# Kernel optimization log

Measured on AMD Instinct MI355X. Metric: run time of the kernel, lower is better.

Reference implementation:

```python
import jax, jax.numpy as jnp
import numpy as np
from jax import lax

N_BOXES = 6000
IOU_THR = 0.5
CONF_THR = 0.6


def setup_inputs() -> dict:
    key = jax.random.key(0)
    k1, k2, k3 = jax.random.split(key, 3)
    # valid xyxy boxes: top-left in [0,1000), width/height in [1,101)
    xy = jax.random.uniform(k1, (N_BOXES, 2), dtype=jnp.float32) * 1000.0
    wh = jax.random.uniform(k2, (N_BOXES, 2), dtype=jnp.float32) * 100.0 + 1.0
    boxes = jnp.concatenate([xy, xy + wh], axis=-1)  # [N,4] x1,y1,x2,y2
    scores = jax.random.uniform(k3, (N_BOXES,), dtype=jnp.float32)
    return {"boxes": boxes, "scores": scores}


def _pairwise_iou(b):
    # b: [N,4] xyxy. Returns [N,N] IoU, coordinates handled separately to
    # avoid materializing [N,N,2] intermediates.
    x1, y1, x2, y2 = b[:, 0], b[:, 1], b[:, 2], b[:, 3]
    area = (x2 - x1) * (y2 - y1)  # [N]
    iw = jnp.clip(jnp.minimum(x2[:, None], x2[None, :]) - jnp.maximum(x1[:, None], x1[None, :]), 0.0)
    ih = jnp.clip(jnp.minimum(y2[:, None], y2[None, :]) - jnp.maximum(y1[:, None], y1[None, :]), 0.0)
    inter = iw * ih  # [N,N]
    return inter / (area[:, None] + area[None, :] - inter)


def reference(boxes, scores):
    """torchvision-style NMS (suppress IoU > 0.5) then confidence filter (>= 0.6).
    Returns masked scores [N]: score where the box survives both stages, else 0.
    (Fixed-shape mask form of the original index outputs, for jit compatibility.)
    """
    n = scores.shape[0]
    order = jnp.argsort(-scores)  # descending by confidence
    iou = _pairwise_iou(boxes[order])  # [N,N] in sorted order
    idx = jnp.arange(n)

    def body(suppressed, i):
        keep_i = jnp.logical_not(suppressed[i])
        # a kept box suppresses all lower-scoring boxes with IoU > threshold
        supp_new = keep_i & (iou[i] > IOU_THR) & (idx > i)
        return suppressed | supp_new, keep_i

    _, keep_sorted = lax.scan(body, jnp.zeros((n,), dtype=bool), idx)
    keep = jnp.zeros((n,), dtype=bool).at[order].set(keep_sorted)
    final = keep & (scores >= CONF_THR)
    return jnp.where(final, scores, 0.0)
```

## Files before the change

kernel.cpp:

```cpp
#include <hip/hip_runtime.h>
#include <stdint.h>

#define N_BOXES 6000
#define NT 94
#define NTP 96
#define NROWS (NTP * 64)
#define CAP 16
#define IOU_THR 0.5f
#define CONF_THR 0.6f

typedef unsigned long long u64;
typedef unsigned int u32;
typedef unsigned short u16;

#define BAR() asm volatile("s_waitcnt lgkmcnt(0)\n\ts_barrier" ::: "memory")

__device__ __forceinline__ u64 rdlane64(u64 v, int l) {
    unsigned lo = (unsigned)__builtin_amdgcn_readlane((int)(unsigned)v, l);
    unsigned hi = (unsigned)__builtin_amdgcn_readlane((int)(unsigned)(v >> 32), l);
    return ((u64)hi << 32) | lo;
}

__global__ void __launch_bounds__(1024) k_sort(const float* __restrict__ scores,
                                               const float4* __restrict__ boxes,
                                               int* __restrict__ sidx,
                                               float4* __restrict__ sboxes,
                                               u32* __restrict__ lists_w,
                                               int* __restrict__ cnt) {
    __shared__ u64 kt[N_BOXES];
    __shared__ int part[1024];
    const int tid = threadIdx.x;
    const int gtid = blockIdx.x * 1024 + tid;
    for (int j = gtid; j < NROWS * CAP / 2; j += NT * 1024) lists_w[j] = 0xFFFFFFFFu;
    for (int j = gtid; j < NROWS; j += NT * 1024) cnt[j] = 0;

    for (int j = tid; j < N_BOXES; j += 1024) {
        unsigned inv = ~__float_as_uint(scores[j]);
        kt[j] = ((u64)inv << 32) | (unsigned)j;
    }
    __syncthreads();
    const int il = tid & 63;
    const int i = blockIdx.x * 64 + il;
    const int j0 = (tid >> 6) * 375;
    u64 mykey = (i < N_BOXES) ? kt[i] : 0ull;
    int cntr = 0;
#pragma unroll 5
    for (int jj = 0; jj < 375; ++jj)
        cntr += (kt[j0 + jj] < mykey) ? 1 : 0;
    part[tid] = cntr;
    __syncthreads();
    if (tid < 64 && i < N_BOXES) {
        int r = 0;
#pragma unroll
        for (int s = 0; s < 16; ++s) r += part[il + 64 * s];
        sidx[r] = i;
        sboxes[r] = boxes[i];
    }
}

__global__ void k_mask(const float4* __restrict__ sboxes,
                       u16* __restrict__ lists, int* __restrict__ cnt,
                       u64* __restrict__ diagw) {
    int ct = blockIdx.x, rt = blockIdx.y;
    if (ct < rt) return;
    int lane = threadIdx.x;
    __shared__ float4 rb[64];
    int row0 = rt * 64;
    int rows = min(64, N_BOXES - row0);
    if (lane < rows) rb[lane] = sboxes[row0 + lane];
    __syncthreads();
    int j = ct * 64 + lane;
    bool jvalid = (j < N_BOXES);
    float4 cb = make_float4(0.f, 0.f, 1.f, 1.f);
    if (jvalid) cb = sboxes[j];
    float carea = (cb.z - cb.x) * (cb.w - cb.y);
    bool isdiag = (ct == rt);
    for (int i = 0; i < rows; ++i) {
        float4 rbx = rb[i];
        float rarea = (rbx.z - rbx.x) * (rbx.w - rbx.y);
        float iw = fmaxf(fminf(rbx.z, cb.z) - fmaxf(rbx.x, cb.x), 0.f);
        float ih = fmaxf(fminf(rbx.w, cb.w) - fmaxf(rbx.y, cb.y), 0.f);
        float inter = iw * ih;
        float iou = inter / ((rarea + carea) - inter);
        int row = row0 + i;
        bool pred = jvalid && (j > row) && (iou > IOU_THR);
        if (isdiag) {
            u64 bal = __ballot(pred);
            if (lane == (i & 63)) diagw[row] = bal;
        } else if (pred) {
            int slot = atomicAdd(&cnt[row], 1);
            if (slot < CAP) lists[row * CAP + slot] = (u16)j;
        }
    }
}

__global__ void __launch_bounds__(256) k_scan(const u16* __restrict__ lists,
                                              const u64* __restrict__ diagw,
                                              const int* __restrict__ sidx,
                                              const float* __restrict__ scores,
                                              float* __restrict__ out) {
    __shared__ u64 removed[NTP];
    __shared__ u64 kwbuf[NTP];
    const int tid   = threadIdx.x;
    const int lane  = tid & 63;
    const int row_l = tid >> 2;
    const int sg    = (tid & 3) * 4;
    if (tid < NTP) removed[tid] = 0;

    u64 L0, L1, L2, D0, D1, D2;
    L0 = *(const u64*)&lists[(0 * 64 + row_l) * CAP + sg];
    L1 = *(const u64*)&lists[(1 * 64 + row_l) * CAP + sg];
    L2 = *(const u64*)&lists[(2 * 64 + row_l) * CAP + sg];
    D0 = diagw[0 * 64 + lane];
    D1 = diagw[1 * 64 + lane];
    D2 = diagw[2 * 64 + lane];
    __syncthreads();

#define STEP(T, LUSE, DUSE)                                                    \
    {                                                                          \
        const u64 nz = __ballot(DUSE != 0ull);        \
        const int row0 = (T) * 64;                                             \
        const int rem = N_BOXES - row0;                                        \
        const u64 valid = (rem >= 64) ? ~0ull                                  \
                        : ((rem <= 0) ? 0ull : ((1ull << rem) - 1ull));        \
        u64 c = valid & ~removed[(T)];                                         \
        u64 kw = 0;                                                            \
        while (c) {                                                            \
            u64 blockers = c & nz;                                             \
            if (!blockers) { kw |= c; break; }             \
            int g = (int)__builtin_ctzll(blockers);                            \
            u64 below = c & ((1ull << g) - 1ull);         \
            kw |= below | (1ull << g);                                         \
            u64 df = rdlane64(DUSE, g);                     \
            c &= ~(df | below | (1ull << g));                                  \
        }                                                                      \
        if (tid == 0) kwbuf[(T)] = kw;                                         \
        if (((kw >> row_l) & 1ull) && LUSE != ~0ull) {                         \
            u16 e0 = (u16)(LUSE), e1 = (u16)(LUSE >> 16),                      \
                e2 = (u16)(LUSE >> 32), e3 = (u16)(LUSE >> 48);                \
            if (e0 != 0xFFFFu) atomicOr(&removed[e0 >> 6], 1ull << (e0 & 63)); \
            if (e1 != 0xFFFFu) atomicOr(&removed[e1 >> 6], 1ull << (e1 & 63)); \
            if (e2 != 0xFFFFu) atomicOr(&removed[e2 >> 6], 1ull << (e2 & 63)); \
            if (e3 != 0xFFFFu) atomicOr(&removed[e3 >> 6], 1ull << (e3 & 63)); \
        }                                                                      \
        const int tn = ((T) + 3 < NTP) ? ((T) + 3) : ((T) + 3 - NTP);          \
        LUSE = *(const u64*)&lists[(tn * 64 + row_l) * CAP + sg];              \
        DUSE = diagw[tn * 64 + lane];                                          \
        BAR();                                                                 \
    }

    for (int t = 0; t < NTP; t += 3) {
        STEP(t,     L0, D0)
        STEP(t + 1, L1, D1)
        STEP(t + 2, L2, D2)
    }
#undef STEP

    for (int p = tid; p < N_BOXES; p += 256) {
        int orig = sidx[p];
        float s = scores[orig];
        bool k = (kwbuf[p >> 6] >> (p & 63)) & 1ull;
        out[orig] = (k && (s >= CONF_THR)) ? s : 0.0f;
    }
}

extern "C" void kernel_launch(void* const* d_in, const int* in_sizes, int n_in,
                              void* d_out, int out_size, void* d_ws, size_t ws_size,
                              hipStream_t stream) {
    const float* boxes  = (const float*)d_in[0];
    const float* scores = (const float*)d_in[1];
    float* out = (float*)d_out;

    char* ws = (char*)d_ws;
    u16*    lists  = (u16*)(ws);
    int*    cnt    = (int*)(ws + 196608);
    u64*    diagw  = (u64*)(ws + 221184);
    int*    sidx   = (int*)(ws + 270336);
    float4* sboxes = (float4*)(ws + 294336);

    k_sort<<<dim3(NT), dim3(1024), 0, stream>>>(scores, (const float4*)boxes, sidx,
                                                sboxes, (u32*)lists, cnt);
    k_mask<<<dim3(NT, NT), dim3(64), 0, stream>>>((const float4*)sboxes, lists, cnt, diagw);
    k_scan<<<dim3(1), dim3(256), 0, stream>>>(lists, diagw, sidx, scores, out);
}
```

Before: 132.8 us.

## Widen scan step to 128-row tiles to halve barrier-separated steps

```diff
diff --git a/kernel.cpp b/kernel.cpp
--- a/kernel.cpp
+++ b/kernel.cpp
@@ -4,6 +4,8 @@
 #define N_BOXES 6000
 #define NT 94
 #define NTP 96
+#define NT2 47
+#define NTP2 48
 #define NROWS (NTP * 64)
 #define CAP 16
 #define IOU_THR 0.5f
@@ -26,13 +28,15 @@
                                                int* __restrict__ sidx,
                                                float4* __restrict__ sboxes,
                                                u32* __restrict__ lists_w,
-                                               int* __restrict__ cnt) {
+                                               int* __restrict__ cnt,
+                                               u64* __restrict__ diagw2) {
     __shared__ u64 kt[N_BOXES];
     __shared__ int part[1024];
     const int tid = threadIdx.x;
     const int gtid = blockIdx.x * 1024 + tid;
     for (int j = gtid; j < NROWS * CAP / 2; j += NT * 1024) lists_w[j] = 0xFFFFFFFFu;
     for (int j = gtid; j < NROWS; j += NT * 1024) cnt[j] = 0;
+    for (int j = gtid; j < NROWS * 2; j += NT * 1024) diagw2[j] = 0ull;
 
     for (int j = tid; j < N_BOXES; j += 1024) {
         unsigned inv = ~__float_as_uint(scores[j]);
@@ -60,7 +64,7 @@
 
 __global__ void k_mask(const float4* __restrict__ sboxes,
                        u16* __restrict__ lists, int* __restrict__ cnt,
-                       u64* __restrict__ diagw) {
+                       u64* __restrict__ diagw2) {
     int ct = blockIdx.x, rt = blockIdx.y;
     if (ct < rt) return;
     int lane = threadIdx.x;
@@ -74,7 +78,8 @@
     float4 cb = make_float4(0.f, 0.f, 1.f, 1.f);
     if (jvalid) cb = sboxes[j];
     float carea = (cb.z - cb.x) * (cb.w - cb.y);
-    bool isdiag = (ct == rt);
+    const bool indiag = ((ct >> 1) == (rt >> 1));
+    const int wi = ct & 1;
     for (int i = 0; i < rows; ++i) {
         float4 rbx = rb[i];
         float rarea = (rbx.z - rbx.x) * (rbx.w - rbx.y);
@@ -84,9 +89,9 @@
         float iou = inter / ((rarea + carea) - inter);
         int row = row0 + i;
         bool pred = jvalid && (j > row) && (iou > IOU_THR);
-        if (isdiag) {
+        if (indiag) {
             u64 bal = __ballot(pred);
-            if (lane == (i & 63)) diagw[row] = bal;
+            if (lane == (i & 63)) diagw2[row * 2 + wi] = bal;
         } else if (pred) {
             int slot = atomicAdd(&cnt[row], 1);
             if (slot < CAP) lists[row * CAP + slot] = (u16)j;
@@ -95,7 +100,7 @@
 }
 
 __global__ void __launch_bounds__(256) k_scan(const u16* __restrict__ lists,
-                                              const u64* __restrict__ diagw,
+                                              const u64* __restrict__ diagw2,
                                               const int* __restrict__ sidx,
                                               const float* __restrict__ scores,
                                               float* __restrict__ out) {
@@ -103,58 +108,83 @@
     __shared__ u64 kwbuf[NTP];
     const int tid   = threadIdx.x;
     const int lane  = tid & 63;
-    const int row_l = tid >> 2;
-    const int sg    = (tid & 3) * 4;
+    const int row_l = tid >> 1;
+    const int sg    = (tid & 1) * 8;
     if (tid < NTP) removed[tid] = 0;
 
-    u64 L0, L1, L2, D0, D1, D2;
-    L0 = *(const u64*)&lists[(0 * 64 + row_l) * CAP + sg];
-    L1 = *(const u64*)&lists[(1 * 64 + row_l) * CAP + sg];
-    L2 = *(const u64*)&lists[(2 * 64 + row_l) * CAP + sg];
-    D0 = diagw[0 * 64 + lane];
-    D1 = diagw[1 * 64 + lane];
-    D2 = diagw[2 * 64 + lane];
-    __syncthreads();
-
-#define STEP(T, LUSE, DUSE)                                                    \
+    uint4 LA0, LA1, LA2;
+    ulonglong2 DAa, DAb, DAc;
+    u64 DBa, DBb, DBc;
+    LA0 = *(const uint4*)&lists[(0 * 128 + row_l) * CAP + sg];
+    LA1 = *(const uint4*)&lists[(1 * 128 + row_l) * CAP + sg];
+    LA2 = *(const uint4*)&lists[(2 * 128 + row_l) * CAP + sg];
+    DAa = *(const ulonglong2*)&diagw2[(0 * 128 + lane) * 2];
+    DAb = *(const ulonglong2*)&diagw2[(1 * 128 + lane) * 2];
+    DAc = *(const ulonglong2*)&diagw2[(2 * 128 + lane) * 2];
+    DBa = diagw2[(0 * 128 + 64 + lane) * 2 + 1];
+    DBb = diagw2[(1 * 128 + 64 + lane) * 2 + 1];
+    DBc = diagw2[(2 * 128 + 64 + lane) * 2 + 1];
+    __syncthreads();
+
+#define SCAT(w)                                                                \
+    {   u32 e0 = (w) & 0xFFFFu, e1 = (w) >> 16;                                \
+        if (e0 != 0xFFFFu) atomicOr(&removed[e0 >> 6], 1ull << (e0 & 63));     \
+        if (e1 != 0xFFFFu) atomicOr(&removed[e1 >> 6], 1ull << (e1 & 63)); }
+
+#define STEP(T, LA, DA, DB)                                                    \
     {                                                                          \
-        const u64 nz = __ballot(DUSE != 0ull);        \
-        const int row0 = (T) * 64;                                             \
-        const int rem = N_BOXES - row0;                                        \
-        const u64 valid = (rem >= 64) ? ~0ull                                  \
-                        : ((rem <= 0) ? 0ull : ((1ull << rem) - 1ull));        \
-        u64 c = valid & ~removed[(T)];                                         \
-        u64 kw = 0;                                                            \
-        while (c) {                                                            \
-            u64 blockers = c & nz;                                             \
-            if (!blockers) { kw |= c; break; }             \
-            int g = (int)__builtin_ctzll(blockers);                            \
-            u64 below = c & ((1ull << g) - 1ull);         \
-            kw |= below | (1ull << g);                                         \
-            u64 df = rdlane64(DUSE, g);                     \
-            c &= ~(df | below | (1ull << g));                                  \
+        const u64 A0 = DA.x, A1 = DA.y;                                        \
+        const u64 nz0 = __ballot((A0 | A1) != 0ull);                           \
+        const u64 nz1 = __ballot(DB != 0ull);                                  \
+        const int rem0 = N_BOXES - (T) * 128;                                  \
+        const int rem1 = rem0 - 64;                                            \
+        const u64 valid0 = (rem0 >= 64) ? ~0ull                                \
+                         : ((rem0 <= 0) ? 0ull : ((1ull << rem0) - 1ull));     \
+        const u64 valid1 = (rem1 >= 64) ? ~0ull                                \
+                         : ((rem1 <= 0) ? 0ull : ((1ull << rem1) - 1ull));     \
+        u64 c0 = valid0 & ~removed[2 * (T)];                                   \
+        u64 c1 = valid1 & ~removed[2 * (T) + 1];                               \
+        u64 kw0 = 0, kw1 = 0;                                                  \
+        while (c0 | c1) {                                                      \
+            u64 b0 = c0 & nz0;                                                 \
+            if (b0) {                                                          \
+                int g = (int)__builtin_ctzll(b0);                              \
+                u64 below = c0 & ((1ull << g) - 1ull);    \
+                kw0 |= below | (1ull << g);                                    \
+                u64 d0 = rdlane64(A0, g);                   \
+                u64 d1 = rdlane64(A1, g);                                      \
+                c0 &= ~(d0 | below | (1ull << g));                             \
+                c1 &= ~d1;                                                     \
+            } else {                                                           \
+                kw0 |= c0; c0 = 0;         \
+                u64 b1 = c1 & nz1;                                             \
+                if (!b1) { kw1 |= c1; break; }             \
+                int g = (int)__builtin_ctzll(b1);                              \
+                u64 below = c1 & ((1ull << g) - 1ull);                         \
+                kw1 |= below | (1ull << g);                                    \
+                u64 d1 = rdlane64(DB, g);                   \
+                c1 &= ~(d1 | below | (1ull << g));                             \
+            }                                                                  \
         }                                                                      \
-        if (tid == 0) kwbuf[(T)] = kw;                                         \
-        if (((kw >> row_l) & 1ull) && LUSE != ~0ull) {                         \
-            u16 e0 = (u16)(LUSE), e1 = (u16)(LUSE >> 16),                      \
-                e2 = (u16)(LUSE >> 32), e3 = (u16)(LUSE >> 48);                \
-            if (e0 != 0xFFFFu) atomicOr(&removed[e0 >> 6], 1ull << (e0 & 63)); \
-            if (e1 != 0xFFFFu) atomicOr(&removed[e1 >> 6], 1ull << (e1 & 63)); \
-            if (e2 != 0xFFFFu) atomicOr(&removed[e2 >> 6], 1ull << (e2 & 63)); \
-            if (e3 != 0xFFFFu) atomicOr(&removed[e3 >> 6], 1ull << (e3 & 63)); \
+        if (tid == 0) { kwbuf[2 * (T)] = kw0; kwbuf[2 * (T) + 1] = kw1; }      \
+        const u64 kws = (row_l < 64) ? kw0 : kw1;                              \
+        if (((kws >> (row_l & 63)) & 1ull) && ((LA.x & 0xFFFFu) != 0xFFFFu)) { \
+            SCAT(LA.x) SCAT(LA.y) SCAT(LA.z) SCAT(LA.w)                        \
         }                                                                      \
-        const int tn = ((T) + 3 < NTP) ? ((T) + 3) : ((T) + 3 - NTP);          \
-        LUSE = *(const u64*)&lists[(tn * 64 + row_l) * CAP + sg];              \
-        DUSE = diagw[tn * 64 + lane];                                          \
+        const int tn = ((T) + 3 < NTP2) ? ((T) + 3) : ((T) + 3 - NTP2);        \
+        LA = *(const uint4*)&lists[(tn * 128 + row_l) * CAP + sg];             \
+        DA = *(const ulonglong2*)&diagw2[(tn * 128 + lane) * 2];               \
+        DB = diagw2[(tn * 128 + 64 + lane) * 2 + 1];                           \
         BAR();                                                                 \
     }
 
-    for (int t = 0; t < NTP; t += 3) {
-        STEP(t,     L0, D0)
-        STEP(t + 1, L1, D1)
-        STEP(t + 2, L2, D2)
+    for (int t = 0; t < NTP2; t += 3) {
+        STEP(t,     LA0, DAa, DBa)
+        STEP(t + 1, LA1, DAb, DBb)
+        STEP(t + 2, LA2, DAc, DBc)
     }
 #undef STEP
+#undef SCAT
 
     for (int p = tid; p < N_BOXES; p += 256) {
         int orig = sidx[p];
@@ -174,12 +204,13 @@
     char* ws = (char*)d_ws;
     u16*    lists  = (u16*)(ws);
     int*    cnt    = (int*)(ws + 196608);
-    u64*    diagw  = (u64*)(ws + 221184);
-    int*    sidx   = (int*)(ws + 270336);
-    float4* sboxes = (float4*)(ws + 294336);
+    u64*    diagw2 = (u64*)(ws + 221184);
+    int*    sidx   = (int*)(ws + 319488);
+    float4* sboxes = (float4*)(ws + 343488);
 
     k_sort<<<dim3(NT), dim3(1024), 0, stream>>>(scores, (const float4*)boxes, sidx,
-                                                sboxes, (u32*)lists, cnt);
-    k_mask<<<dim3(NT, NT), dim3(64), 0, stream>>>((const float4*)sboxes, lists, cnt, diagw);
-    k_scan<<<dim3(1), dim3(256), 0, stream>>>(lists, diagw, sidx, scores, out);
-}
+                                                sboxes, (u32*)lists, cnt, diagw2);
+    k_mask<<<dim3(NT, NT), dim3(64), 0, stream>>>((const float4*)sboxes, lists, cnt,
+                                                  diagw2);
+    k_scan<<<dim3(1), dim3(256), 0, stream>>>(lists, diagw2, sidx, scores, out);
+}
```

Measured after the change: 130.1 us. 1.02x faster.
